# Kernel optimization log

Measured on AMD Instinct MI355X. Metric: run time of the kernel, lower is better.

## Reference

```python
import jax, jax.numpy as jnp
import numpy as np

H = 1024  # hidden_dim
NEG_INF = -1e10


def setup_inputs() -> dict:
    key = jax.random.key(0)
    k1, k2, k3, k4, k5 = jax.random.split(key, 5)
    B, L = 16, 2048
    encoder_out = jax.random.normal(k1, (B, L, 2 * H), dtype=jnp.float32)
    mask = jax.random.randint(k2, (B, L), 0, 2, dtype=jnp.int32)
    v = jax.random.normal(k3, (1, B, H), dtype=jnp.float32)
    attn_w = jax.random.normal(k4, (H, 3 * H), dtype=jnp.float32) * 0.02
    attn_b = jnp.zeros((H,), dtype=jnp.float32)
    v_w = jax.random.normal(k5, (1, H), dtype=jnp.float32) * 0.02
    return {"encoder_out": encoder_out, "mask": mask, "v": v,
            "attn_w": attn_w, "attn_b": attn_b, "v_w": v_w}


def reference(encoder_out, mask, v, attn_w, attn_b, v_w):
    # Original: en = Linear(cat(v_rep, encoder_out)); split the weight instead
    # of materializing the [B, L, 3H] concat (same math).
    W_v = attn_w[:, :H]        # [H, H]   acts on the repeated decoder state
    W_e = attn_w[:, H:]        # [H, 2H]  acts on encoder outputs
    dec = v[0]                 # [B, H]  (transpose(0,1) then squeeze of repeat)
    score_dec = dec @ W_v.T + attn_b                      # [B, H]
    score_enc = jnp.einsum('ble,he->blh', encoder_out, W_e)  # [B, L, H]
    en = jnp.tanh(score_dec[:, None, :] + score_enc)       # [B, L, H]
    attention = jnp.einsum('blh,h->bl', en, v_w[0])         # [B, L]
    attention = jnp.where(mask == 0, NEG_INF, attention)
    return jax.nn.softmax(attention, axis=1)
```

## Files before the change

### kernel.cpp

```cpp
#include <hip/hip_runtime.h>
#include <stdint.h>

#define LSEQ 2048
#define M_TOT 32768
#define KDIM 2048
#define NKT 64
#define NCT 4
#define NEG_INF_F (-10000000000.0f)

typedef _Float16 f16;
typedef f16 f16x8 __attribute__((ext_vector_type(8)));
typedef float f32x4 __attribute__((ext_vector_type(4)));

#define WS_SDEC_OFF  0
#define WS_PART_OFF  (64u << 10)
#define WS_POS_OFF   (576u << 10)
#define WS_RIDX_OFF  (704u << 10)
#define WS_NKEEP_OFF (832u << 10)
#define WS_WET_OFF   (2u << 20)

#define A_OFF(s) ((s) * 8192)
#define B_OFF(s) (16384 + (s) * 16384)

__device__ inline void gload16(const void* g, void* l) {
    __builtin_amdgcn_global_load_lds(
        (const __attribute__((address_space(1))) void*)g,
        (__attribute__((address_space(3))) void*)l, 16, 0, 0);
}

__device__ inline float tanh_mul(float x, float s) {
    float ax = __builtin_fabsf(x);
    float e  = __expf(-2.f * ax);
    float th = (1.f - e) * __builtin_amdgcn_rcpf(1.f + e);
    float sv = __uint_as_float(__float_as_uint(s) ^ (__float_as_uint(x) & 0x80000000u));
    return th * sv;
}

__global__ __launch_bounds__(256) void prep_kernel(
        const float* __restrict__ attn_w, f16* __restrict__ weT,
        const float* __restrict__ v, const float* __restrict__ attn_b,
        float* __restrict__ sdec,
        const int* __restrict__ mask, int* __restrict__ ridx,
        int* __restrict__ pos, int* __restrict__ nkeep) {
    const int blk = blockIdx.x;
    const int tid = threadIdx.x;
    __shared__ int wsum[4];

    if (blk < 256) {
        int g = blk * 1024 + tid;
        #pragma unroll
        for (int q = 0; q < 4; ++q, g += 256) {
            int ct  = g >> 16;
            int rem = g & 65535;
            int kt  = rem >> 10;
            int p   = rem & 1023;
            int row = p >> 2;
            int sl  = (p & 3) ^ ((row >> 1) & 3);
            const float* s = attn_w + (size_t)(ct * 256 + row) * 3072 + 1024 + kt * 32 + sl * 8;
            float4 a = *(const float4*)s;
            float4 b = *(const float4*)(s + 4);
            f16x8 h = { (f16)a.x,(f16)a.y,(f16)a.z,(f16)a.w,(f16)b.x,(f16)b.y,(f16)b.z,(f16)b.w };
            *(f16x8*)(weT + (size_t)g * 8) = h;
        }
    } else if (blk < 1280) {
        const int wave = (blk - 256) * 4 + (tid >> 6);
        const int lane = tid & 63;
        #pragma unroll
        for (int i = 0; i < 4; ++i) {
            const int gid = wave * 4 + i;
            const int b = gid >> 10;
            const int h = gid & 1023;
            const float* vr = v + b * 1024;
            const float* wr = attn_w + (size_t)h * 3072;
            float s = 0.f;
            #pragma unroll 4
            for (int k = lane; k < 1024; k += 64) s += vr[k] * wr[k];
            #pragma unroll
            for (int m = 1; m < 64; m <<= 1) s += __shfl_xor(s, m);
            if (lane == 0) sdec[b * 1024 + h] = s + attn_b[h];
        }
    } else {
        const int b = blk - 1280;
        const int lane = tid & 63, w = tid >> 6;
        const int base = b * 2048 + tid * 8;
        int m[8], cnt = 0;
        #pragma unroll
        for (int i = 0; i < 8; ++i) { m[i] = mask[base + i] != 0; cnt += m[i]; }
        int inc = cnt;
        #pragma unroll
        for (int d = 1; d < 64; d <<= 1) {
            int t = __shfl_up(inc, d);
            if (lane >= d) inc += t;
        }
        if (lane == 63) wsum[w] = inc;
        __syncthreads();
        int wbase = 0, total = 0;
        #pragma unroll
        for (int i = 0; i < 4; ++i) { if (i < w) wbase += wsum[i]; total += wsum[i]; }
        int p = wbase + inc - cnt;
        #pragma unroll
        for (int i = 0; i < 8; ++i) {
            if (m[i]) { ridx[b * 2048 + p] = base + i; pos[base + i] = p; p++; }
            else      { pos[base + i] = -1; }
        }
        if (tid == 0) nkeep[b] = total;
    }
}

#define PH_OPEN  do { __builtin_amdgcn_sched_barrier(0); __builtin_amdgcn_s_barrier(); \
                      asm volatile("s_waitcnt lgkmcnt(0)" ::: "memory"); \
                      __builtin_amdgcn_sched_barrier(0); } while (0)
#define PH_CLOSE do { __builtin_amdgcn_sched_barrier(0); __builtin_amdgcn_s_barrier(); } while (0)

__global__ __launch_bounds__(256, 2) void fused_gemm(
        const float* __restrict__ enc,
        const f16* __restrict__ weT,
        const float* __restrict__ sdec,
        const float* __restrict__ vw,
        const int* __restrict__ ridx,
        const int* __restrict__ nkeep,
        float* __restrict__ part)
{
    const int logical = ((int)blockIdx.x & 7) * 128 + ((int)blockIdx.x >> 3);
    const int rt = logical >> 2;
    const int ct = logical & 3;

    const int b  = rt >> 4;
    const int rl = rt & 15;
    const int nk = nkeep[b];
    if (rl * 128 >= nk) return;

    const int tid = threadIdx.x;
    const int l15 = tid & 15;
    const int l4  = (tid >> 4) & 3;
    const int wv  = tid >> 6;
    const int wm  = wv >> 1;
    const int wn  = wv & 1;

    __shared__ char lds[65536];
    __shared__ float red[2][128];

    const char* bT = (const char*)weT + ((size_t)ct << 20);

    const int ar_ = tid >> 1;
    const int ah  = tid & 1;
    int cidx = rl * 128 + ar_;
    if (cidx >= nk) cidx = rl * 128;
    const int grow = ridx[b * 2048 + cidx];
    const float* aG = enc + (size_t)grow * KDIM + ah * 16;
    const int aswz = (ar_ >> 1) & 3;
    const int awb0 = ar_ * 64 + (((2 * ah)     ^ aswz) << 4);
    const int awb1 = ar_ * 64 + (((2 * ah + 1) ^ aswz) << 4);

    const int fswz = (l4 ^ ((l15 >> 1) & 3)) << 4;
    const int aro = (wm * 64  + l15) * 64 + fswz;
    const int bro = (wn * 128 + l15) * 64 + fswz;

    f32x4 acc[4][8] = {};

    auto loadAreg = [&](float4 (&s)[4], int t) {
        const float* p = aG + (size_t)t * 32;
        s[0] = *(const float4*)(p);
        s[1] = *(const float4*)(p + 4);
        s[2] = *(const float4*)(p + 8);
        s[3] = *(const float4*)(p + 12);
    };
    auto writeA = [&](const float4 (&s)[4], int slot) {
        char* d = lds + A_OFF(slot);
        auto c0 = __builtin_amdgcn_cvt_pkrtz(s[0].x, s[0].y);
        auto c1 = __builtin_amdgcn_cvt_pkrtz(s[0].z, s[0].w);
        auto c2 = __builtin_amdgcn_cvt_pkrtz(s[1].x, s[1].y);
        auto c3 = __builtin_amdgcn_cvt_pkrtz(s[1].z, s[1].w);
        auto c4 = __builtin_amdgcn_cvt_pkrtz(s[2].x, s[2].y);
        auto c5 = __builtin_amdgcn_cvt_pkrtz(s[2].z, s[2].w);
        auto c6 = __builtin_amdgcn_cvt_pkrtz(s[3].x, s[3].y);
        auto c7 = __builtin_amdgcn_cvt_pkrtz(s[3].z, s[3].w);
        f16x8 h0 = { (f16)c0[0],(f16)c0[1],(f16)c1[0],(f16)c1[1],
                     (f16)c2[0],(f16)c2[1],(f16)c3[0],(f16)c3[1] };
        f16x8 h1 = { (f16)c4[0],(f16)c4[1],(f16)c5[0],(f16)c5[1],
                     (f16)c6[0],(f16)c6[1],(f16)c7[0],(f16)c7[1] };
        *(f16x8*)(d + awb0) = h0;
        *(f16x8*)(d + awb1) = h1;
    };
    auto stageB = [&](int t, int slot) {
        const char* s = bT + ((size_t)t << 14) + tid * 16;
        char* d = lds + B_OFF(slot) + tid * 16;
        gload16(s, d);               gload16(s + 4096, d + 4096);
        gload16(s + 8192, d + 8192); gload16(s + 12288, d + 12288);
    };

    int brS = 0, bwS = 2;

    auto body = [&](int t, float4 (&sIss)[4], float4 (&sCvt)[4]) {
        const char* sa = lds + A_OFF(t & 1);
        const char* sb = lds + B_OFF(brS);
        f16x8 fa[4], bf[4];
        #pragma unroll
        for (int ii = 0; ii < 4; ++ii) fa[ii] = *(const f16x8*)(sa + aro + ii * 1024);
        #pragma unroll
        for (int j = 0; j < 4; ++j)  bf[j]  = *(const f16x8*)(sb + bro + j * 1024);
        if (t + 2 < NKT) loadAreg(sIss, t + 2);
        PH_OPEN;
        __builtin_amdgcn_s_setprio(1);
        #pragma unroll
        for (int ii = 0; ii < 4; ++ii)
            #pragma unroll
            for (int j = 0; j < 4; ++j)
                acc[ii][j] = __builtin_amdgcn_mfma_f32_16x16x32_f16(fa[ii], bf[j], acc[ii][j], 0, 0, 0);
        __builtin_amdgcn_s_setprio(0);
        PH_CLOSE;
        #pragma unroll
        for (int j = 0; j < 4; ++j) bf[j] = *(const f16x8*)(sb + bro + (4 + j) * 1024);
        if (t + 1 < NKT) writeA(sCvt, (t + 1) & 1);
        if (t + 2 < NKT) stageB(t + 2, bwS);
        PH_OPEN;
        __builtin_amdgcn_s_setprio(1);
        #pragma unroll
        for (int ii = 0; ii < 4; ++ii)
            #pragma unroll
            for (int j = 0; j < 4; ++j)
                acc[ii][4 + j] = __builtin_amdgcn_mfma_f32_16x16x32_f16(fa[ii], bf[j], acc[ii][4 + j], 0, 0, 0);
        __builtin_amdgcn_s_setprio(0);
        if (t < NKT - 2) { asm volatile("s_waitcnt vmcnt(8)" ::: "memory"); }
        else             { asm volatile("s_waitcnt vmcnt(0)" ::: "memory"); }
        PH_CLOSE;
        brS = (brS == 2) ? 0 : brS + 1;
        bwS = (bwS == 2) ? 0 : bwS + 1;
    };

    float4 sEven[4], sOdd[4];
    loadAreg(sEven, 0);
    writeA(sEven, 0);
    loadAreg(sOdd, 1);
    stageB(0, 0); stageB(1, 1);
    asm volatile("s_waitcnt lgkmcnt(0)" ::: "memory");
    asm volatile("s_waitcnt vmcnt(4)" ::: "memory");
    __builtin_amdgcn_s_barrier();
    __builtin_amdgcn_sched_barrier(0);

    #pragma unroll 1
    for (int tt = 0; tt < NKT; tt += 2) {
        body(tt,     sEven, sOdd);
        body(tt + 1, sOdd,  sEven);
    }

    const int colbase = ct * 256;

    float sd[8], vs[8];
    #pragma unroll
    for (int j = 0; j < 8; ++j) {
        const int col = colbase + wn * 128 + j * 16 + l15;
        sd[j] = sdec[b * 1024 + col];
        vs[j] = vw[col];
    }
    float psum[4][4] = {};
    #pragma unroll
    for (int i = 0; i < 4; ++i)
        #pragma unroll
        for (int j = 0; j < 8; ++j)
            #pragma unroll
            for (int q = 0; q < 4; ++q)
                psum[i][q] += tanh_mul(acc[i][j][q] + sd[j], vs[j]);

    #pragma unroll
    for (int i = 0; i < 4; ++i)
        #pragma unroll
        for (int q = 0; q < 4; ++q) {
            float s = psum[i][q];
            s += __shfl_xor(s, 1); s += __shfl_xor(s, 2);
            s += __shfl_xor(s, 4); s += __shfl_xor(s, 8);
            psum[i][q] = s;
        }

    __syncthreads();
    if (l15 == 0) {
        #pragma unroll
        for (int i = 0; i < 4; ++i)
            #pragma unroll
            for (int q = 0; q < 4; ++q)
                red[wn][wm * 64 + i * 16 + l4 * 4 + q] = psum[i][q];
    }
    __syncthreads();
    if (tid < 128)
        part[(size_t)ct * M_TOT + b * 2048 + rl * 128 + tid] =
            red[0][tid] + red[1][tid];
}

__global__ __launch_bounds__(512) void softmax_kernel(
        const float* __restrict__ part, const int* __restrict__ pos,
        float* __restrict__ out) {
    int b = blockIdx.x;
    int tid = threadIdx.x;
    int lane = tid & 63, w = tid >> 6;
    __shared__ float sred[8];

    float vals[4];
    #pragma unroll
    for (int p = 0; p < 4; ++p) {
        int row = b * LSEQ + tid + p * 512;
        int pp = pos[row];
        float val = NEG_INF_F;
        if (pp >= 0) {
            int crow = b * 2048 + pp;
            val = 0.f;
            #pragma unroll
            for (int q = 0; q < NCT; ++q) val += part[(size_t)q * M_TOT + crow];
        }
        vals[p] = val;
    }
    float mx = fmaxf(fmaxf(vals[0], vals[1]), fmaxf(vals[2], vals[3]));
    #pragma unroll
    for (int m = 1; m < 64; m <<= 1) mx = fmaxf(mx, __shfl_xor(mx, m));
    if (lane == 0) sred[w] = mx;
    __syncthreads();
    float gmax = sred[0];
    #pragma unroll
    for (int i = 1; i < 8; ++i) gmax = fmaxf(gmax, sred[i]);

    float es[4]; float ssum = 0.f;
    #pragma unroll
    for (int p = 0; p < 4; ++p) { es[p] = expf(vals[p] - gmax); ssum += es[p]; }
    #pragma unroll
    for (int m = 1; m < 64; m <<= 1) ssum += __shfl_xor(ssum, m);
    __syncthreads();
    if (lane == 0) sred[w] = ssum;
    __syncthreads();
    float gsum = 0.f;
    #pragma unroll
    for (int i = 0; i < 8; ++i) gsum += sred[i];
    float inv = 1.f / gsum;
    #pragma unroll
    for (int p = 0; p < 4; ++p)
        out[b * LSEQ + tid + p * 512] = es[p] * inv;
}

extern "C" void kernel_launch(void* const* d_in, const int* in_sizes, int n_in,
                              void* d_out, int out_size, void* d_ws, size_t ws_size,
                              hipStream_t stream) {
    const float* enc    = (const float*)d_in[0];
    const int*   mask   = (const int*)  d_in[1];
    const float* v      = (const float*)d_in[2];
    const float* attn_w = (const float*)d_in[3];
    const float* attn_b = (const float*)d_in[4];
    const float* v_w    = (const float*)d_in[5];
    float* out = (float*)d_out;

    char* ws = (char*)d_ws;
    float* sdec  = (float*)(ws + WS_SDEC_OFF);
    float* part  = (float*)(ws + WS_PART_OFF);
    int*   pos   = (int*)  (ws + WS_POS_OFF);
    int*   ridx  = (int*)  (ws + WS_RIDX_OFF);
    int*   nkeep = (int*)  (ws + WS_NKEEP_OFF);
    f16*   weT   = (f16*)  (ws + WS_WET_OFF);

    hipLaunchKernelGGL(prep_kernel,    dim3(1296), dim3(256), 0, stream,
                       attn_w, weT, v, attn_b, sdec, mask, ridx, pos, nkeep);
    hipLaunchKernelGGL(fused_gemm,     dim3(1024), dim3(256), 0, stream,
                       enc, weT, sdec, v_w, ridx, nkeep, part);
    hipLaunchKernelGGL(softmax_kernel, dim3(16),   dim3(512), 0, stream, part, pos, out);
}
```

Before: 134.2 us.

## Compact masked rows globally across batches instead of per batch

```diff
diff --git a/kernel.cpp b/kernel.cpp
--- a/kernel.cpp
+++ b/kernel.cpp
@@ -62,30 +62,32 @@
             f16x8 h = { (f16)a.x,(f16)a.y,(f16)a.z,(f16)a.w,(f16)b.x,(f16)b.y,(f16)b.z,(f16)b.w };
             *(f16x8*)(weT + (size_t)g * 8) = h;
         }
-    } else if (blk < 1280) {
-        const int wave = (blk - 256) * 4 + (tid >> 6);
+    } else if (blk < 512) {
+        const int h = (blk - 256) * 4 + (tid >> 6);
         const int lane = tid & 63;
-        #pragma unroll
-        for (int i = 0; i < 4; ++i) {
-            const int gid = wave * 4 + i;
-            const int b = gid >> 10;
-            const int h = gid & 1023;
-            const float* vr = v + b * 1024;
-            const float* wr = attn_w + (size_t)h * 3072;
-            float s = 0.f;
-            #pragma unroll 4
-            for (int k = lane; k < 1024; k += 64) s += vr[k] * wr[k];
-            #pragma unroll
-            for (int m = 1; m < 64; m <<= 1) s += __shfl_xor(s, m);
-            if (lane == 0) sdec[b * 1024 + h] = s + attn_b[h];
+        const float* wr = attn_w + (size_t)h * 3072;
+        float s[16];
+        #pragma unroll
+        for (int b = 0; b < 16; ++b) s[b] = 0.f;
+        for (int k = 0; k < 16; ++k) {
+            const int idx = lane + 64 * k;
+            const float w_ = wr[idx];
+            #pragma unroll
+            for (int b = 0; b < 16; ++b) s[b] += v[b * 1024 + idx] * w_;
+        }
+        const float bias = attn_b[h];
+        #pragma unroll
+        for (int b = 0; b < 16; ++b) {
+            float t = s[b];
+            #pragma unroll
+            for (int m = 1; m < 64; m <<= 1) t += __shfl_xor(t, m);
+            if (lane == 0) sdec[b * 1024 + h] = t + bias;
         }
     } else {
-        const int b = blk - 1280;
         const int lane = tid & 63, w = tid >> 6;
-        const int base = b * 2048 + tid * 8;
-        int m[8], cnt = 0;
-        #pragma unroll
-        for (int i = 0; i < 8; ++i) { m[i] = mask[base + i] != 0; cnt += m[i]; }
+        const int base = tid * 128;
+        int cnt = 0;
+        for (int i = 0; i < 128; ++i) cnt += (mask[base + i] != 0);
         int inc = cnt;
         #pragma unroll
         for (int d = 1; d < 64; d <<= 1) {
@@ -98,12 +100,12 @@
         #pragma unroll
         for (int i = 0; i < 4; ++i) { if (i < w) wbase += wsum[i]; total += wsum[i]; }
         int p = wbase + inc - cnt;
-        #pragma unroll
-        for (int i = 0; i < 8; ++i) {
-            if (m[i]) { ridx[b * 2048 + p] = base + i; pos[base + i] = p; p++; }
-            else      { pos[base + i] = -1; }
-        }
-        if (tid == 0) nkeep[b] = total;
+        for (int i = 0; i < 128; ++i) {
+            const int r = base + i;
+            if (mask[r] != 0) { ridx[p] = r; pos[r] = p; p++; }
+            else              { pos[r] = -1; }
+        }
+        if (tid == 0) nkeep[0] = total;
     }
 }
 
@@ -121,14 +123,13 @@
         const int* __restrict__ nkeep,
         float* __restrict__ part)
 {
-    const int logical = ((int)blockIdx.x & 7) * 128 + ((int)blockIdx.x >> 3);
-    const int rt = logical >> 2;
-    const int ct = logical & 3;
-
-    const int b  = rt >> 4;
-    const int rl = rt & 15;
-    const int nk = nkeep[b];
-    if (rl * 128 >= nk) return;
+    const int lg = ((int)blockIdx.x & 7) * 128 + ((int)blockIdx.x >> 3);
+    const int i4 = lg >> 2;
+    const int ct = lg & 3;
+    const int rt = ((i4 & 31) << 3) + (i4 >> 5);
+
+    const int nk = nkeep[0];
+    if (rt * 128 >= nk) return;
 
     const int tid = threadIdx.x;
     const int l15 = tid & 15;
@@ -139,14 +140,15 @@
 
     __shared__ char lds[65536];
     __shared__ float red[2][128];
+    __shared__ int bArr[128];
 
     const char* bT = (const char*)weT + ((size_t)ct << 20);
 
     const int ar_ = tid >> 1;
     const int ah  = tid & 1;
-    int cidx = rl * 128 + ar_;
-    if (cidx >= nk) cidx = rl * 128;
-    const int grow = ridx[b * 2048 + cidx];
+    int cidx = rt * 128 + ar_;
+    if (cidx >= nk) cidx = rt * 128;
+    const int grow = ridx[cidx];
     const float* aG = enc + (size_t)grow * KDIM + ah * 16;
     const int aswz = (ar_ >> 1) & 3;
     const int awb0 = ar_ * 64 + (((2 * ah)     ^ aswz) << 4);
@@ -246,21 +248,32 @@
 
     const int colbase = ct * 256;
 
-    float sd[8], vs[8];
+    __syncthreads();
+    if (tid < 128) {
+        int ci = rt * 128 + tid;
+        if (ci >= nk) ci = rt * 128;
+        bArr[tid] = ridx[ci] >> 11;
+    }
+    __syncthreads();
+
+    float vs[8];
+    int colv[8];
     #pragma unroll
     for (int j = 0; j < 8; ++j) {
-        const int col = colbase + wn * 128 + j * 16 + l15;
-        sd[j] = sdec[b * 1024 + col];
-        vs[j] = vw[col];
+        colv[j] = colbase + wn * 128 + j * 16 + l15;
+        vs[j] = vw[colv[j]];
     }
     float psum[4][4] = {};
     #pragma unroll
     for (int i = 0; i < 4; ++i)
         #pragma unroll
-        for (int j = 0; j < 8; ++j)
-            #pragma unroll
-            for (int q = 0; q < 4; ++q)
-                psum[i][q] += tanh_mul(acc[i][j][q] + sd[j], vs[j]);
+        for (int q = 0; q < 4; ++q) {
+            const int b_ = bArr[wm * 64 + i * 16 + l4 * 4 + q];
+            const float* sdr = sdec + b_ * 1024;
+            #pragma unroll
+            for (int j = 0; j < 8; ++j)
+                psum[i][q] += tanh_mul(acc[i][j][q] + sdr[colv[j]], vs[j]);
+        }
 
     #pragma unroll
     for (int i = 0; i < 4; ++i)
@@ -282,8 +295,7 @@
     }
     __syncthreads();
     if (tid < 128)
-        part[(size_t)ct * M_TOT + b * 2048 + rl * 128 + tid] =
-            red[0][tid] + red[1][tid];
+        part[(size_t)ct * M_TOT + rt * 128 + tid] = red[0][tid] + red[1][tid];
 }
 
 __global__ __launch_bounds__(512) void softmax_kernel(
@@ -301,10 +313,9 @@
         int pp = pos[row];
         float val = NEG_INF_F;
         if (pp >= 0) {
-            int crow = b * 2048 + pp;
             val = 0.f;
             #pragma unroll
-            for (int q = 0; q < NCT; ++q) val += part[(size_t)q * M_TOT + crow];
+            for (int q = 0; q < NCT; ++q) val += part[(size_t)q * M_TOT + pp];
         }
         vals[p] = val;
     }
@@ -353,7 +364,7 @@
     int*   nkeep = (int*)  (ws + WS_NKEEP_OFF);
     f16*   weT   = (f16*)  (ws + WS_WET_OFF);
 
-    hipLaunchKernelGGL(prep_kernel,    dim3(1296), dim3(256), 0, stream,
+    hipLaunchKernelGGL(prep_kernel,    dim3(513),  dim3(256), 0, stream,
                        attn_w, weT, v, attn_b, sdec, mask, ridx, pos, nkeep);
     hipLaunchKernelGGL(fused_gemm,     dim3(1024), dim3(256), 0, stream,
                        enc, weT, sdec, v_w, ridx, nkeep, part);
```

Measured after the change: 187.2 us. 1.4x slower.
